# Kernel optimization log

Hardware: AMD Instinct MI355X
Metric: run time of the kernel (lower is better)

## Reference

```python
import jax, jax.numpy as jnp
import numpy as np

N_NODES = 100_000
N_EDGES = 1_600_000
N_GRAPHS = 512
HID = 64
NUM_CLASSES = 100
VOCAB = 3100
ID_OFFSET = 1500
BN_EPS = 1e-5


def setup_inputs() -> dict:
    key = jax.random.key(0)
    ks = jax.random.split(key, 8)
    node_ids = jax.random.randint(ks[0], (N_NODES,), 0, 1600)
    edge_src = jax.random.randint(ks[1], (N_EDGES,), 0, N_NODES)
    edge_dst = jax.random.randint(ks[2], (N_EDGES,), 0, N_NODES)
    graph_ids = jnp.sort(jax.random.randint(ks[3], (N_NODES,), 0, N_GRAPHS))
    emb = jax.random.normal(ks[4], (VOCAB, HID), dtype=jnp.float32) * 0.02
    # 3 GIN layers x 3 MLP linear layers, all 64->64 since embedding_dim == hidden
    Ws = jax.random.normal(ks[5], (3, 3, HID, HID), dtype=jnp.float32) * 0.05
    bs = jnp.zeros((3, 3, HID), dtype=jnp.float32)
    bn_gamma = jnp.ones((3, HID), dtype=jnp.float32)
    bn_beta = jnp.zeros((3, HID), dtype=jnp.float32)
    eps = jnp.zeros((3,), dtype=jnp.float32)  # learn_eps=True, init 0
    W_out = jax.random.normal(ks[6], (3 * HID, NUM_CLASSES), dtype=jnp.float32) * 0.05
    b_out = jnp.zeros((NUM_CLASSES,), dtype=jnp.float32)
    return {"node_ids": node_ids, "edge_src": edge_src, "edge_dst": edge_dst,
            "graph_ids": graph_ids, "emb": emb, "Ws": Ws, "bs": bs,
            "bn_gamma": bn_gamma, "bn_beta": bn_beta, "eps": eps,
            "W_out": W_out, "b_out": b_out}


def reference(node_ids, edge_src, edge_dst, graph_ids, emb, Ws, bs,
              bn_gamma, bn_beta, eps, W_out, b_out):
    n = node_ids.shape[0]
    h = emb[node_ids + ID_OFFSET]  # [N, HID]
    pooled = []
    for l in range(3):  # GIN layers (fixed small count)
        # GINConv, sum aggregator: (1+eps)*h + sum over in-edges of h[src]
        agg = jax.ops.segment_sum(h[edge_src], edge_dst, num_segments=n)
        x = (1.0 + eps[l]) * h + agg
        for m in range(3):
            x = jax.nn.relu(x @ Ws[l, m] + bs[l, m])
        mean = x.mean(axis=0)
        var = x.var(axis=0)  # biased var, as torch BN uses for normalization
        x = (x - mean) * jax.lax.rsqrt(var + BN_EPS) * bn_gamma[l] + bn_beta[l]
        h = x
        # dgl.sum_nodes: per-graph segment sum
        pooled.append(jax.ops.segment_sum(h, graph_ids, num_segments=N_GRAPHS))
    graph_features = jnp.concatenate(pooled, axis=-1)  # [G, 3*HID]
    return graph_features @ W_out + b_out  # [G, NUM_CLASSES]
```

## Files before the change

kernel.cpp:

```cpp
#include <hip/hip_runtime.h>

#define N_NODES 100000
#define N_EDGES 1600000
#define N_GRAPHS 512
#define HID 64
#define NUM_CLASSES 100
#define ID_OFFSET 1500
#define BN_EPS 1e-5f
#define CAP 64
#define NBKT 256
#define BSHIFT 9
#define NUSED ((N_NODES + 511) >> 9)
#define BCAP 10240
#define CBLK 98
#define CHUNK 16384
#define WPBLK 5
#define EMBBLK ((N_NODES * 32 + 1023) / 1024)
#define DUMMY_ROW 100000

typedef __attribute__((ext_vector_type(8))) short short8;
typedef __attribute__((ext_vector_type(4))) float floatx4;

__device__ __forceinline__ float b2f(unsigned short u) {
    return __builtin_bit_cast(float, ((unsigned)u) << 16);
}
__device__ __forceinline__ unsigned short f2b(float f) {
    unsigned x = __builtin_bit_cast(unsigned, f);
    x += 0x7FFFu + ((x >> 16) & 1u);
    return (unsigned short)(x >> 16);
}

#define XSH(row, qq) ((((((row) >> 4) << 7) + ((qq) << 4) + (((row) & 15) ^ (qq))) * 8))


__global__ __launch_bounds__(1024) void prep_kernel(const int* __restrict__ src,
                                                    const int* __restrict__ dst,
                                                    int* __restrict__ cursor,
                                                    int* __restrict__ rec,
                                                    const float* __restrict__ Ws,
                                                    unsigned short* __restrict__ whi,
                                                    unsigned short* __restrict__ wlo,
                                                    const int* __restrict__ node_ids,
                                                    const int* __restrict__ gid,
                                                    const float* __restrict__ emb,
                                                    unsigned short* __restrict__ h,
                                                    int* __restrict__ gs,
                                                    int* __restrict__ ge) {
    __shared__ int hist[NBKT];
    __shared__ int base_s[NBKT];
    int t = threadIdx.x;
    int blk = blockIdx.x;

    if (blk < CBLK) {
        if (t < NBKT) hist[t] = 0;
        __syncthreads();
        int cb = blk * CHUNK;
        int d_[16], s_[16];
#pragma unroll
        for (int k = 0; k < 16; ++k) {
            int i = cb + k * 1024 + t;
            d_[k] = (i < N_EDGES) ? dst[i] : -1;
            s_[k] = (i < N_EDGES) ? src[i] : 0;
            if (d_[k] >= 0) atomicAdd(&hist[((unsigned)d_[k] >> BSHIFT) & (NBKT - 1)], 1);
        }
        __syncthreads();
        if (t < NBKT) base_s[t] = (hist[t] > 0) ? atomicAdd(&cursor[t], hist[t]) : 0;
        __syncthreads();
        if (t < NBKT) hist[t] = 0;
        __syncthreads();
#pragma unroll
        for (int k = 0; k < 16; ++k) {
            if (d_[k] >= 0) {
                unsigned d = (unsigned)d_[k];
                int b = (d >> BSHIFT) & (NBKT - 1);
                int p = atomicAdd(&hist[b], 1);
                int g = base_s[b] + p;
                if ((unsigned)g < BCAP)
                    rec[b * BCAP + g] = ((int)(d & 511) << 17) | (s_[k] & 0x1FFFF);
            }
        }
    } else if (blk < CBLK + WPBLK) {
        int G = (blk - CBLK) * 1024 + t;
        if (G < 3 * 1536) {
            int l = G / 1536, Gp = G % 1536;
            int mm = Gp >> 9, rem = Gp & 511;
            int kq = rem >> 6, n = rem & 63;
            const float* Wp = Ws + l * 12288 + mm * 4096 + (kq * 8) * 64 + n;
            unsigned short uh[8], ul[8];
#pragma unroll
            for (int j = 0; j < 8; ++j) {
                float w = Wp[j * 64];
                unsigned short hi = f2b(w);
                uh[j] = hi;
                ul[j] = f2b(w - b2f(hi));
            }
            size_t off = (size_t)l * 12288 + (mm << 12) + XSH(n, kq);
            *(short8*)&whi[off] = *(short8*)uh;
            *(short8*)&wlo[off] = *(short8*)ul;
        }
    } else {
        int idx = (blk - CBLK - WPBLK) * 1024 + t;
        if (idx < N_NODES * 32) {
            int n = idx >> 5, cp = idx & 31;
            const float2 e = *(const float2*)(emb + (((size_t)(node_ids[n] + ID_OFFSET)) << 6) + cp * 2);
            unsigned v = (unsigned)f2b(e.x) | ((unsigned)f2b(e.y) << 16);
            ((unsigned*)h)[n * 32 + cp] = v;
            if (cp == 0) {
                int g = gid[n] & (N_GRAPHS - 1);
                if (n == 0 || (gid[n - 1] & (N_GRAPHS - 1)) != g) gs[g] = n;
                if (n == N_NODES - 1 || (gid[n + 1] & (N_GRAPHS - 1)) != g) ge[g] = n + 1;
            }
        }
    }
}


__global__ __launch_bounds__(1024) void fill_kernel(const int* __restrict__ rec,
                                                    const int* __restrict__ cursor,
                                                    int* __restrict__ cnt,
                                                    int* __restrict__ srcs) {
    __shared__ int lcnt[512];
    int t = threadIdx.x;
    int b = blockIdx.x;
    if (t < 512) lcnt[t] = 0;
    __syncthreads();
    int nb = cursor[b];
    if (nb < 0) nb = 0;
    if (nb > BCAP) nb = BCAP;
    const int* seg = rec + b * BCAP;
    for (int i = t; i < nb; i += 1024) {
        unsigned r = (unsigned)seg[i];
        int dl = (int)((r >> 17) & 511);
        int s = (int)(r & 0x1FFFF);
        int node = (b << BSHIFT) + dl;
        int p = atomicAdd(&lcnt[dl], 1);
        if (p < CAP && node < N_NODES) srcs[(node << 6) + p] = s;
    }
    __syncthreads();
    if (t < 512) {
        int node = (b << BSHIFT) + t;
        if (node < N_NODES) {
            int deg = lcnt[t];
            cnt[node] = deg;
            int degc = deg > CAP ? CAP : deg;
            int degp = (degc + 15) & ~15;
            if (degp < 16) degp = 16;
            for (int p = degc; p < degp; ++p) srcs[(node << 6) + p] = DUMMY_ROW;
        }
    }
}


__global__ __launch_bounds__(256) void agg_kernel(const unsigned short* __restrict__ x,
                                                  const int* __restrict__ cnt,
                                                  const int* __restrict__ srcs,
                                                  const float* __restrict__ eps, int l,
                                                  const float* __restrict__ stats,
                                                  const float* __restrict__ gamma,
                                                  const float* __restrict__ beta,
                                                  unsigned short* __restrict__ out) {
    int nb = __builtin_amdgcn_readfirstlane(((blockIdx.x << 2) + (threadIdx.x >> 6)) << 2);
    int lane = threadIdx.x & 63;
    int half = lane >> 5;
    int cl = lane & 31;
    const unsigned* __restrict__ xu = (const unsigned*)x;

    float scale = 1.0f + eps[l];
    float a0f = 1.0f, a1f = 1.0f, b0f = 0.0f, b1f = 0.0f;
    if (l > 0) {
        int lp = l - 1;
        float2 sm = *(const float2*)&stats[lp * 128 + 2 * cl];
        float2 sq = *(const float2*)&stats[lp * 128 + 64 + 2 * cl];
        float2 gm = *(const float2*)&gamma[lp * 64 + 2 * cl];
        float2 bt = *(const float2*)&beta[lp * 64 + 2 * cl];
        float mean0 = sm.x * (1.0f / N_NODES);
        float var0 = sq.x * (1.0f / N_NODES) - mean0 * mean0;
        float r0 = rsqrtf(var0 + BN_EPS);
        a0f = gm.x * r0;
        b0f = bt.x - mean0 * a0f;
        float mean1 = sm.y * (1.0f / N_NODES);
        float var1 = sq.y * (1.0f / N_NODES) - mean1 * mean1;
        float r1 = rsqrtf(var1 + BN_EPS);
        a1f = gm.y * r1;
        b1f = bt.y - mean1 * a1f;
    }

    int deg[4], degp[4];
    const int* row[4];
#pragma unroll
    for (int n = 0; n < 4; ++n) {
        int d = cnt[nb + n];
        int dc = d < 0 ? 0 : (d > CAP ? CAP : d);
        deg[n] = dc;
        int dp = (dc + 15) & ~15;
        degp[n] = dp < 16 ? 16 : dp;
        row[n] = srcs + ((size_t)(nb + n) << 6);
    }
    int cmax = degp[0];
    cmax = degp[1] > cmax ? degp[1] : cmax;
    cmax = degp[2] > cmax ? degp[2] : cmax;
    cmax = degp[3] > cmax ? degp[3] : cmax;

    unsigned us[4];
#pragma unroll
    for (int n = 0; n < 4; ++n) us[n] = xu[(size_t)(nb + n) * 32 + cl];

    float A0[4] = {0.f, 0.f, 0.f, 0.f}, A1[4] = {0.f, 0.f, 0.f, 0.f};
    float B0[4] = {0.f, 0.f, 0.f, 0.f}, B1[4] = {0.f, 0.f, 0.f, 0.f};

    {
        unsigned uv[4][8];
#pragma unroll
        for (int n = 0; n < 4; ++n)
#pragma unroll
            for (int k = 0; k < 8; ++k) {
                int ia = row[n][2 * k] & 0x1FFFF;
                int ib = row[n][2 * k + 1] & 0x1FFFF;
                int idx = half ? ib : ia;
                uv[n][k] = xu[(size_t)idx * 32 + cl];
            }
#pragma unroll
        for (int n = 0; n < 4; ++n)
#pragma unroll
            for (int k = 0; k < 8; ++k) {
                float lo = b2f((unsigned short)(uv[n][k] & 0xFFFF));
                float hi = b2f((unsigned short)(uv[n][k] >> 16));
                if (k & 1) { B0[n] += lo; B1[n] += hi; }
                else       { A0[n] += lo; A1[n] += hi; }
            }
    }

    for (int c = 16; c < cmax; c += 16) {
        unsigned uc[4][8];
#pragma unroll
        for (int n = 0; n < 4; ++n)
            if (c < degp[n])
#pragma unroll
                for (int k = 0; k < 8; ++k) {
                    int ia = row[n][c + 2 * k] & 0x1FFFF;
                    int ib = row[n][c + 2 * k + 1] & 0x1FFFF;
                    int idx = half ? ib : ia;
                    uc[n][k] = xu[(size_t)idx * 32 + cl];
                }
#pragma unroll
        for (int n = 0; n < 4; ++n)
            if (c < degp[n])
#pragma unroll
                for (int k = 0; k < 8; ++k) {
                    float lo = b2f((unsigned short)(uc[n][k] & 0xFFFF));
                    float hi = b2f((unsigned short)(uc[n][k] >> 16));
                    if (k & 1) { B0[n] += lo; B1[n] += hi; }
                    else       { A0[n] += lo; A1[n] += hi; }
                }
    }

#pragma unroll
    for (int n = 0; n < 4; ++n) {
        float S0 = (A0[n] + B0[n]);
        float S1 = (A1[n] + B1[n]);
        S0 += __shfl_xor(S0, 32);
        S1 += __shfl_xor(S1, 32);
        if (half == 0) {
            float selflo = b2f((unsigned short)(us[n] & 0xFFFF));
            float selfhi = b2f((unsigned short)(us[n] >> 16));
            float db = scale + (float)deg[n];
            float v0 = fmaf(a0f, fmaf(scale, selflo, S0), db * b0f);
            float v1 = fmaf(a1f, fmaf(scale, selfhi, S1), db * b1f);
            ((unsigned*)out)[(size_t)(nb + n) * 32 + cl] =
                (unsigned)f2b(v0) | ((unsigned)f2b(v1) << 16);
        }
    }
}


__global__ __launch_bounds__(256, 4) void mlp_kernel(unsigned short* __restrict__ x,
                                                     const unsigned short* __restrict__ whi,
                                                     const unsigned short* __restrict__ wlo,
                                                     const float* __restrict__ bs, int l,
                                                     float* __restrict__ stats,
                                                     const int* __restrict__ graph_ids,
                                                     float* __restrict__ pooled, int last) {
    __shared__ __align__(16) unsigned short xs[128 * 64];
    __shared__ int garr[128];
    __shared__ float ssum[256], sqq[256];
    int t = threadIdx.x;
    int nodebase = blockIdx.x * 128;
    int lane = t & 63, w = t >> 6;

    if (lane < 32) {
        int n = nodebase + w * 32 + lane;
        garr[w * 32 + lane] = (n < N_NODES) ? (graph_ids[n] & (N_GRAPHS - 1)) : -1;
    }
#pragma unroll
    for (int i = 0; i < 4; ++i) {
        int g = i * 64 + lane;
        int rl = g >> 3, qr = g & 7;
        int row = w * 32 + rl;
        const int4 v = *(const int4*)(x + (((size_t)(nodebase + row)) << 6) + qr * 8);
        *(int4*)&xs[XSH(row, qr)] = v;
    }

    int m = lane & 15, q = lane >> 4;
    const float* bb = bs + l * 3 * 64;
    const unsigned short* whil = whi + (size_t)l * 12288;
    const unsigned short* wlol = wlo + (size_t)l * 12288;
    for (int mm = 0; mm < 3; ++mm) {
        short8 bl[2][4];
#pragma unroll
        for (int kc = 0; kc < 2; ++kc)
#pragma unroll
            for (int tj = 0; tj < 4; ++tj)
                bl[kc][tj] = *(const short8*)&wlol[(mm << 12) + XSH(tj * 16 + m, kc * 4 + q)];
        short8 a[2][2];
#pragma unroll
        for (int kc = 0; kc < 2; ++kc)
#pragma unroll
            for (int ti = 0; ti < 2; ++ti)
                a[kc][ti] = *(const short8*)&xs[XSH(w * 32 + ti * 16 + m, kc * 4 + q)];

        floatx4 acc[2][4];
#pragma unroll
        for (int tj = 0; tj < 4; ++tj) {
            float bv = bb[mm * 64 + tj * 16 + m];
#pragma unroll
            for (int ti = 0; ti < 2; ++ti)
                acc[ti][tj] = (floatx4){bv, bv, bv, bv};
        }
#pragma unroll
        for (int kc = 0; kc < 2; ++kc) {
            short8 bh[4];
#pragma unroll
            for (int tj = 0; tj < 4; ++tj)
                bh[tj] = *(const short8*)&whil[(mm << 12) + XSH(tj * 16 + m, kc * 4 + q)];
#pragma unroll
            for (int ti = 0; ti < 2; ++ti)
#pragma unroll
                for (int tj = 0; tj < 4; ++tj)
                    acc[ti][tj] = __builtin_amdgcn_mfma_f32_16x16x32_bf16(a[kc][ti], bh[tj], acc[ti][tj], 0, 0, 0);
        }
#pragma unroll
        for (int kc = 0; kc < 2; ++kc)
#pragma unroll
            for (int ti = 0; ti < 2; ++ti)
#pragma unroll
                for (int tj = 0; tj < 4; ++tj)
                    acc[ti][tj] = __builtin_amdgcn_mfma_f32_16x16x32_bf16(a[kc][ti], bl[kc][tj], acc[ti][tj], 0, 0, 0);
#pragma unroll
        for (int ti = 0; ti < 2; ++ti)
#pragma unroll
            for (int tj = 0; tj < 4; ++tj) {
                int col = tj * 16 + m;
#pragma unroll
                for (int r = 0; r < 4; ++r) {
                    int row = w * 32 + ti * 16 + q * 4 + r;
                    float v = acc[ti][tj][r];
                    xs[XSH(row, col >> 3) + (col & 7)] = f2b(v > 0.f ? v : 0.f);
                }
            }
    }

    if (!last) {
        unsigned* xo = (unsigned*)x;
#pragma unroll
        for (int it = 0; it < 16; ++it) {
            int row = w * 32 + (lane >> 5) + it * 2;
            int cp = lane & 31;
            int col = cp * 2;
            unsigned val = *(const unsigned*)&xs[XSH(row, col >> 3) + (col & 7)];
            int node = nodebase + row;
            if (node < N_NODES) xo[(size_t)node * 32 + cp] = val;
        }
    }
    {
        int c = lane;
        float s = 0.f, q2 = 0.f, acc2 = 0.f;
        int cur = -1;
        for (int k = 0; k < 32; ++k) {
            int row = w * 32 + k;
            int g = garr[row];
            if (g >= 0) {
                float v = b2f(xs[XSH(row, c >> 3) + (c & 7)]);
                s += v;
                q2 += v * v;
                if (g != cur) {
                    if (cur >= 0) atomicAdd(&pooled[cur * 192 + l * 64 + c], acc2);
                    acc2 = 0.f;
                    cur = g;
                }
                acc2 += v;
            }
        }
        if (cur >= 0) atomicAdd(&pooled[cur * 192 + l * 64 + c], acc2);
        ssum[t] = s;
        sqq[t] = q2;
    }
    __syncthreads();
    if (t < 64) {
        float S = ssum[t] + ssum[t + 64] + ssum[t + 128] + ssum[t + 192];
        float Q = sqq[t] + sqq[t + 64] + sqq[t + 128] + sqq[t + 192];
        atomicAdd(&stats[l * 128 + t], S);
        atomicAdd(&stats[l * 128 + 64 + t], Q);
    }
}


__global__ __launch_bounds__(256) void out_kernel(const float* __restrict__ pooled,
                                                  const float* __restrict__ stats,
                                                  const float* __restrict__ gamma,
                                                  const float* __restrict__ beta,
                                                  const int* __restrict__ gs,
                                                  const int* __restrict__ ge,
                                                  const float* __restrict__ Wo,
                                                  const float* __restrict__ bo,
                                                  float* __restrict__ out) {
    __shared__ float sab[384];
    int t = threadIdx.x;
    if (t < 192) {
        int l2 = t / 64, c = t & 63;
        float mean = stats[l2 * 128 + c] * (1.0f / N_NODES);
        float var = stats[l2 * 128 + 64 + c] * (1.0f / N_NODES) - mean * mean;
        float rstd = rsqrtf(var + BN_EPS);
        float a = gamma[l2 * 64 + c] * rstd;
        sab[l2 * 128 + c] = a;
        sab[l2 * 128 + 64 + c] = beta[l2 * 64 + c] - mean * a;
    }
    __syncthreads();
    int idx = blockIdx.x * blockDim.x + t;
    if (idx < N_GRAPHS * NUM_CLASSES) {
        int g = idx / NUM_CLASSES, k = idx % NUM_CLASSES;
        float cg = (float)(ge[g] - gs[g]);
        float acc = bo[k];
        for (int l2 = 0; l2 < 3; ++l2)
            for (int c = 0; c < 64; ++c) {
                float gf = fmaf(sab[l2 * 128 + c], pooled[g * 192 + l2 * 64 + c],
                                sab[l2 * 128 + 64 + c] * cg);
                acc = fmaf(gf, Wo[(l2 * 64 + c) * NUM_CLASSES + k], acc);
            }
        out[idx] = acc;
    }
}

extern "C" void kernel_launch(void* const* d_in, const int* in_sizes, int n_in,
                              void* d_out, int out_size, void* d_ws, size_t ws_size,
                              hipStream_t stream) {
    const int*   node_ids  = (const int*)d_in[0];
    const int*   edge_src  = (const int*)d_in[1];
    const int*   edge_dst  = (const int*)d_in[2];
    const int*   graph_ids = (const int*)d_in[3];
    const float* emb       = (const float*)d_in[4];
    const float* Ws        = (const float*)d_in[5];
    const float* bs        = (const float*)d_in[6];
    const float* gamma     = (const float*)d_in[7];
    const float* beta      = (const float*)d_in[8];
    const float* eps       = (const float*)d_in[9];
    const float* W_out     = (const float*)d_in[10];
    const float* b_out     = (const float*)d_in[11];
    float* out = (float*)d_out;

    unsigned short* h    = (unsigned short*)d_ws;
    unsigned short* xin  = h + 6400000 + 8192;
    unsigned short* whi  = xin + 6400000 + 8192;
    unsigned short* wlo  = whi + 36864;
    int*   srcs   = (int*)(wlo + 36864);
    int*   rec    = srcs + 6400000;
    float* pooled = (float*)(rec + NUSED * BCAP);
    float* stats  = pooled + 98304;
    int*   cnt    = (int*)(stats + 384);
    int*   gs     = cnt + 100000;
    int*   ge     = gs + 512;
    int*   cursor = ge + 512;

    hipMemsetAsync(pooled, 0,
                   (size_t)(98304 + 384 + 100000 + 512 + 512 + 256) * 4, stream);
    hipMemsetAsync(h + (size_t)DUMMY_ROW * 64, 0, 128, stream);
    hipMemsetAsync(xin + (size_t)DUMMY_ROW * 64, 0, 128, stream);

    prep_kernel<<<CBLK + WPBLK + EMBBLK, 1024, 0, stream>>>(
        edge_src, edge_dst, cursor, rec, Ws, whi, wlo,
        node_ids, graph_ids, emb, h, gs, ge);
    fill_kernel<<<NUSED, 1024, 0, stream>>>(rec, cursor, cnt, srcs);

    const int MLP_BLK = (N_NODES + 127) / 128;
    const int AGG_BLK = N_NODES / 16;
    for (int l = 0; l < 3; ++l) {
        unsigned short* X = (l % 2 == 0) ? h : xin;
        unsigned short* A = (l % 2 == 0) ? xin : h;
        agg_kernel<<<AGG_BLK, 256, 0, stream>>>(X, cnt, srcs, eps, l, stats, gamma, beta, A);
        mlp_kernel<<<MLP_BLK, 256, 0, stream>>>(A, whi, wlo, bs, l, stats, graph_ids, pooled, l == 2);
    }

    out_kernel<<<(N_GRAPHS * NUM_CLASSES + 255) / 256, 256, 0, stream>>>(
        pooled, stats, gamma, beta, gs, ge, W_out, b_out, out);
}
```

Baseline: 339.9 us.

## Fuse neighbor aggregation into MLP kernel via shared-memory staging

Merges the per-layer aggregation kernel and the MLP kernel into one kernel. Each 128-node block gathers the neighbor sums itself, with each wave handling 32 nodes in groups of 4, and writes the result straight into the swizzled shared tile the MFMA MLP reads. This removes one global write and read of the aggregated activations per layer, plus three kernel launches. The dummy-row memsets move into the prep kernel. The trade-offs are a long serial gather loop per wave before the matmul, and fewer nodes in flight per wave, which could reduce latency hiding for the random gathers.

```diff
diff --git a/kernel.cpp b/kernel.cpp
--- a/kernel.cpp
+++ b/kernel.cpp
@@ -44,6 +44,7 @@
                                                     const int* __restrict__ gid,
                                                     const float* __restrict__ emb,
                                                     unsigned short* __restrict__ h,
+                                                    unsigned short* __restrict__ xin,
                                                     int* __restrict__ gs,
                                                     int* __restrict__ ge) {
     __shared__ int hist[NBKT];
@@ -52,6 +53,10 @@
     int blk = blockIdx.x;
 
     if (blk < CBLK) {
+        if (blk == 0 && t < 32) {
+            ((unsigned*)(h + (size_t)DUMMY_ROW * 64))[t] = 0u;
+            ((unsigned*)(xin + (size_t)DUMMY_ROW * 64))[t] = 0u;
+        }
         if (t < NBKT) hist[t] = 0;
         __syncthreads();
         int cb = blk * CHUNK;
@@ -151,19 +156,32 @@
 }
 
 
-__global__ __launch_bounds__(256) void agg_kernel(const unsigned short* __restrict__ x,
-                                                  const int* __restrict__ cnt,
-                                                  const int* __restrict__ srcs,
-                                                  const float* __restrict__ eps, int l,
-                                                  const float* __restrict__ stats,
-                                                  const float* __restrict__ gamma,
-                                                  const float* __restrict__ beta,
-                                                  unsigned short* __restrict__ out) {
-    int nb = __builtin_amdgcn_readfirstlane(((blockIdx.x << 2) + (threadIdx.x >> 6)) << 2);
-    int lane = threadIdx.x & 63;
-    int half = lane >> 5;
-    int cl = lane & 31;
+__global__ __launch_bounds__(256, 3) void fused_kernel(const unsigned short* __restrict__ x,
+                                                       unsigned short* __restrict__ xo,
+                                                       const int* __restrict__ cnt,
+                                                       const int* __restrict__ srcs,
+                                                       const float* __restrict__ eps, int l,
+                                                       float* __restrict__ stats,
+                                                       const float* __restrict__ gamma,
+                                                       const float* __restrict__ beta,
+                                                       const unsigned short* __restrict__ whi,
+                                                       const unsigned short* __restrict__ wlo,
+                                                       const float* __restrict__ bs,
+                                                       const int* __restrict__ graph_ids,
+                                                       float* __restrict__ pooled, int last) {
+    __shared__ __align__(16) unsigned short xs[128 * 64];
+    __shared__ int garr[128];
+    __shared__ float ssum[256], sqq[256];
+    int t = threadIdx.x;
+    int nodebase = blockIdx.x * 128;
+    int lane = t & 63, w = t >> 6;
+    int half = lane >> 5, cl = lane & 31;
     const unsigned* __restrict__ xu = (const unsigned*)x;
+
+    if (lane < 32) {
+        int n = nodebase + w * 32 + lane;
+        garr[w * 32 + lane] = (n < N_NODES) ? (graph_ids[n] & (N_GRAPHS - 1)) : -1;
+    }
 
     float scale = 1.0f + eps[l];
     float a0f = 1.0f, a1f = 1.0f, b0f = 0.0f, b1f = 0.0f;
@@ -185,119 +203,96 @@
         b1f = bt.y - mean1 * a1f;
     }
 
-    int deg[4], degp[4];
-    const int* row[4];
-#pragma unroll
-    for (int n = 0; n < 4; ++n) {
-        int d = cnt[nb + n];
-        int dc = d < 0 ? 0 : (d > CAP ? CAP : d);
-        deg[n] = dc;
-        int dp = (dc + 15) & ~15;
-        degp[n] = dp < 16 ? 16 : dp;
-        row[n] = srcs + ((size_t)(nb + n) << 6);
-    }
-    int cmax = degp[0];
-    cmax = degp[1] > cmax ? degp[1] : cmax;
-    cmax = degp[2] > cmax ? degp[2] : cmax;
-    cmax = degp[3] > cmax ? degp[3] : cmax;
-
-    unsigned us[4];
-#pragma unroll
-    for (int n = 0; n < 4; ++n) us[n] = xu[(size_t)(nb + n) * 32 + cl];
-
-    float A0[4] = {0.f, 0.f, 0.f, 0.f}, A1[4] = {0.f, 0.f, 0.f, 0.f};
-    float B0[4] = {0.f, 0.f, 0.f, 0.f}, B1[4] = {0.f, 0.f, 0.f, 0.f};
-
-    {
-        unsigned uv[4][8];
-#pragma unroll
-        for (int n = 0; n < 4; ++n)
-#pragma unroll
-            for (int k = 0; k < 8; ++k) {
-                int ia = row[n][2 * k] & 0x1FFFF;
-                int ib = row[n][2 * k + 1] & 0x1FFFF;
-                int idx = half ? ib : ia;
-                uv[n][k] = xu[(size_t)idx * 32 + cl];
-            }
-#pragma unroll
-        for (int n = 0; n < 4; ++n)
-#pragma unroll
-            for (int k = 0; k < 8; ++k) {
-                float lo = b2f((unsigned short)(uv[n][k] & 0xFFFF));
-                float hi = b2f((unsigned short)(uv[n][k] >> 16));
-                if (k & 1) { B0[n] += lo; B1[n] += hi; }
-                else       { A0[n] += lo; A1[n] += hi; }
-            }
-    }
-
-    for (int c = 16; c < cmax; c += 16) {
-        unsigned uc[4][8];
-#pragma unroll
-        for (int n = 0; n < 4; ++n)
-            if (c < degp[n])
+    int wb = __builtin_amdgcn_readfirstlane(nodebase + w * 32);
+
+    for (int g4 = 0; g4 < 8; ++g4) {
+        int nb = wb + g4 * 4;
+        int deg[4], degp[4];
+        const int* row[4];
+#pragma unroll
+        for (int n = 0; n < 4; ++n) {
+            int d = (nb + n < N_NODES) ? cnt[nb + n] : 0;
+            int dc = d < 0 ? 0 : (d > CAP ? CAP : d);
+            deg[n] = dc;
+            int dp = (dc + 15) & ~15;
+            degp[n] = dp < 16 ? 16 : dp;
+            row[n] = srcs + ((size_t)(nb + n) << 6);
+        }
+        int cmax = degp[0];
+        cmax = degp[1] > cmax ? degp[1] : cmax;
+        cmax = degp[2] > cmax ? degp[2] : cmax;
+        cmax = degp[3] > cmax ? degp[3] : cmax;
+
+        unsigned us[4];
+#pragma unroll
+        for (int n = 0; n < 4; ++n) us[n] = xu[(size_t)(nb + n) * 32 + cl];
+
+        float A0[4] = {0.f, 0.f, 0.f, 0.f}, A1[4] = {0.f, 0.f, 0.f, 0.f};
+        float B0[4] = {0.f, 0.f, 0.f, 0.f}, B1[4] = {0.f, 0.f, 0.f, 0.f};
+
+        {
+            unsigned uv[4][8];
+#pragma unroll
+            for (int n = 0; n < 4; ++n)
 #pragma unroll
                 for (int k = 0; k < 8; ++k) {
-                    int ia = row[n][c + 2 * k] & 0x1FFFF;
-                    int ib = row[n][c + 2 * k + 1] & 0x1FFFF;
+                    int ia = row[n][2 * k] & 0x1FFFF;
+                    int ib = row[n][2 * k + 1] & 0x1FFFF;
                     int idx = half ? ib : ia;
-                    uc[n][k] = xu[(size_t)idx * 32 + cl];
+                    uv[n][k] = xu[(size_t)idx * 32 + cl];
                 }
 #pragma unroll
-        for (int n = 0; n < 4; ++n)
-            if (c < degp[n])
+            for (int n = 0; n < 4; ++n)
 #pragma unroll
                 for (int k = 0; k < 8; ++k) {
-                    float lo = b2f((unsigned short)(uc[n][k] & 0xFFFF));
-                    float hi = b2f((unsigned short)(uc[n][k] >> 16));
+                    float lo = b2f((unsigned short)(uv[n][k] & 0xFFFF));
+                    float hi = b2f((unsigned short)(uv[n][k] >> 16));
                     if (k & 1) { B0[n] += lo; B1[n] += hi; }
                     else       { A0[n] += lo; A1[n] += hi; }
                 }
-    }
-
-#pragma unroll
-    for (int n = 0; n < 4; ++n) {
-        float S0 = (A0[n] + B0[n]);
-        float S1 = (A1[n] + B1[n]);
-        S0 += __shfl_xor(S0, 32);
-        S1 += __shfl_xor(S1, 32);
-        if (half == 0) {
-            float selflo = b2f((unsigned short)(us[n] & 0xFFFF));
-            float selfhi = b2f((unsigned short)(us[n] >> 16));
-            float db = scale + (float)deg[n];
-            float v0 = fmaf(a0f, fmaf(scale, selflo, S0), db * b0f);
-            float v1 = fmaf(a1f, fmaf(scale, selfhi, S1), db * b1f);
-            ((unsigned*)out)[(size_t)(nb + n) * 32 + cl] =
-                (unsigned)f2b(v0) | ((unsigned)f2b(v1) << 16);
-        }
-    }
-}
-
-
-__global__ __launch_bounds__(256, 4) void mlp_kernel(unsigned short* __restrict__ x,
-                                                     const unsigned short* __restrict__ whi,
-                                                     const unsigned short* __restrict__ wlo,
-                                                     const float* __restrict__ bs, int l,
-                                                     float* __restrict__ stats,
-                                                     const int* __restrict__ graph_ids,
-                                                     float* __restrict__ pooled, int last) {
-    __shared__ __align__(16) unsigned short xs[128 * 64];
-    __shared__ int garr[128];
-    __shared__ float ssum[256], sqq[256];
-    int t = threadIdx.x;
-    int nodebase = blockIdx.x * 128;
-    int lane = t & 63, w = t >> 6;
-
-    if (lane < 32) {
-        int n = nodebase + w * 32 + lane;
-        garr[w * 32 + lane] = (n < N_NODES) ? (graph_ids[n] & (N_GRAPHS - 1)) : -1;
-    }
-#pragma unroll
-    for (int i = 0; i < 4; ++i) {
-        int g = i * 64 + lane;
-        int rl = g >> 3, qr = g & 7;
-        int row = w * 32 + rl;
-        const int4 v = *(const int4*)(x + (((size_t)(nodebase + row)) << 6) + qr * 8);
-        *(int4*)&xs[XSH(row, qr)] = v;
+        }
+        for (int c = 16; c < cmax; c += 16) {
+            unsigned uc[4][8];
+#pragma unroll
+            for (int n = 0; n < 4; ++n)
+                if (c < degp[n])
+#pragma unroll
+                    for (int k = 0; k < 8; ++k) {
+                        int ia = row[n][c + 2 * k] & 0x1FFFF;
+                        int ib = row[n][c + 2 * k + 1] & 0x1FFFF;
+                        int idx = half ? ib : ia;
+                        uc[n][k] = xu[(size_t)idx * 32 + cl];
+                    }
+#pragma unroll
+            for (int n = 0; n < 4; ++n)
+                if (c < degp[n])
+#pragma unroll
+                    for (int k = 0; k < 8; ++k) {
+                        float lo = b2f((unsigned short)(uc[n][k] & 0xFFFF));
+                        float hi = b2f((unsigned short)(uc[n][k] >> 16));
+                        if (k & 1) { B0[n] += lo; B1[n] += hi; }
+                        else       { A0[n] += lo; A1[n] += hi; }
+                    }
+        }
+
+#pragma unroll
+        for (int n = 0; n < 4; ++n) {
+            float S0 = A0[n] + B0[n];
+            float S1 = A1[n] + B1[n];
+            S0 += __shfl_xor(S0, 32);
+            S1 += __shfl_xor(S1, 32);
+            if (half == 0) {
+                float selflo = b2f((unsigned short)(us[n] & 0xFFFF));
+                float selfhi = b2f((unsigned short)(us[n] >> 16));
+                float db = scale + (float)deg[n];
+                float v0 = fmaf(a0f, fmaf(scale, selflo, S0), db * b0f);
+                float v1 = fmaf(a1f, fmaf(scale, selfhi, S1), db * b1f);
+                int r = w * 32 + g4 * 4 + n;
+                int col = 2 * cl;
+                *(unsigned*)&xs[XSH(r, col >> 3) + (col & 7)] =
+                    (unsigned)f2b(v0) | ((unsigned)f2b(v1) << 16);
+            }
+        }
     }
 
     int m = lane & 15, q = lane >> 4;
@@ -360,7 +355,7 @@
     }
 
     if (!last) {
-        unsigned* xo = (unsigned*)x;
+        unsigned* xou = (unsigned*)xo;
 #pragma unroll
         for (int it = 0; it < 16; ++it) {
             int row = w * 32 + (lane >> 5) + it * 2;
@@ -368,7 +363,7 @@
             int col = cp * 2;
             unsigned val = *(const unsigned*)&xs[XSH(row, col >> 3) + (col & 7)];
             int node = nodebase + row;
-            if (node < N_NODES) xo[(size_t)node * 32 + cp] = val;
+            if (node < N_NODES) xou[(size_t)node * 32 + cp] = val;
         }
     }
     {
@@ -472,21 +467,19 @@
 
     hipMemsetAsync(pooled, 0,
                    (size_t)(98304 + 384 + 100000 + 512 + 512 + 256) * 4, stream);
-    hipMemsetAsync(h + (size_t)DUMMY_ROW * 64, 0, 128, stream);
-    hipMemsetAsync(xin + (size_t)DUMMY_ROW * 64, 0, 128, stream);
 
     prep_kernel<<<CBLK + WPBLK + EMBBLK, 1024, 0, stream>>>(
         edge_src, edge_dst, cursor, rec, Ws, whi, wlo,
-        node_ids, graph_ids, emb, h, gs, ge);
+        node_ids, graph_ids, emb, h, xin, gs, ge);
     fill_kernel<<<NUSED, 1024, 0, stream>>>(rec, cursor, cnt, srcs);
 
-    const int MLP_BLK = (N_NODES + 127) / 128;
-    const int AGG_BLK = N_NODES / 16;
+    const int FUSE_BLK = (N_NODES + 127) / 128;
     for (int l = 0; l < 3; ++l) {
-        unsigned short* X = (l % 2 == 0) ? h : xin;
+        const unsigned short* X = (l % 2 == 0) ? h : xin;
         unsigned short* A = (l % 2 == 0) ? xin : h;
-        agg_kernel<<<AGG_BLK, 256, 0, stream>>>(X, cnt, srcs, eps, l, stats, gamma, beta, A);
-        mlp_kernel<<<MLP_BLK, 256, 0, stream>>>(A, whi, wlo, bs, l, stats, graph_ids, pooled, l == 2);
+        fused_kernel<<<FUSE_BLK, 256, 0, stream>>>(
+            X, A, cnt, srcs, eps, l, stats, gamma, beta,
+            whi, wlo, bs, graph_ids, pooled, l == 2);
     }
 
     out_kernel<<<(N_GRAPHS * NUM_CLASSES + 255) / 256, 256, 0, stream>>>(
```

Measured after the change: 334.3 us. About the same (-1.6%).
